# Kernel optimization log

Hardware: AMD Instinct MI355X
Metric: run time of the kernel (lower is better)

Reference implementation:

```python
import jax, jax.numpy as jnp
import numpy as np

EPS = 1e-10
TWO_PI = 2.0 * np.pi


def _nll(y_target, o_pred):
    # getCoef: split last dim of o_pred into 5 bivariate-Gaussian params
    mux = o_pred[..., 0]
    muy = o_pred[..., 1]
    sx = jnp.exp(o_pred[..., 2])
    sy = jnp.exp(o_pred[..., 3])
    corr = jnp.tanh(o_pred[..., 4])

    norm_x = (y_target[..., 1] - mux) / sx
    norm_y = (y_target[..., 2] - muy) / sy
    z = norm_x ** 2 + norm_y ** 2 - 2.0 * corr * norm_x * norm_y
    onemrho = 1.0 - corr ** 2
    top = jnp.exp(-z / (2.0 * onemrho))
    bottom = TWO_PI * (sx * sy * jnp.sqrt(onemrho))
    pdf = top / bottom  # (B, T, P)

    # sum over all (b, t, p) of -log(clamp(pdf, eps)), divided by ped_num
    total = jnp.sum(-jnp.log(jnp.clip(pdf, EPS)))
    return total / pdf.shape[2]


def setup_inputs() -> dict:
    key = jax.random.key(0)
    k1, k2 = jax.random.split(key)
    B, T, P = 64, 128, 512
    y_target = jax.random.normal(k1, (B, T, P, 3), dtype=jnp.float32)
    o_pred = jax.random.normal(k2, (B, T, P, 5), dtype=jnp.float32)
    return {"y_target": y_target, "o_pred": o_pred}


def reference(y_target, o_pred):
    return _nll(y_target, o_pred)
```

## Files before the change

kernel.cpp:

```cpp
#include <hip/hip_runtime.h>
#include <hip/hip_bf16.h>


#define THREADS 256
#define PPT 4
#define TILE (THREADS * PPT)

typedef float v4 __attribute__((ext_vector_type(4)));

__device__ __forceinline__ float point_nll(float mux, float muy, float lsx,
                                           float lsy, float w, float y1, float y2) {
    const float LOG_2PI = 1.8378770664093453f;
    const float CLIP    = 23.025850929940457f;
    float isx  = __expf(-lsx);
    float isy  = __expf(-lsy);
    float nx   = (y1 - mux) * isx;
    float ny   = (y2 - muy) * isy;
    float e2w  = __expf(2.0f * w);
    float corr = fmaf(-2.0f, __builtin_amdgcn_rcpf(e2w + 1.0f), 1.0f);
    float omr  = fmaf(-corr, corr, 1.0f);
    float z    = fmaf(nx, nx, ny * ny) - 2.0f * corr * nx * ny;
    float nll  = fmaf(z, 0.5f * __builtin_amdgcn_rcpf(omr),
                      fmaf(0.5f, __logf(omr), lsx + lsy + LOG_2PI));
    return fminf(nll, CLIP);
}

__global__ __launch_bounds__(THREADS) void nll_partial_kernel(
    const float* __restrict__ y, const float* __restrict__ o,
    float* __restrict__ partial, int N) {
    __shared__ v4 lds_o[5 * THREADS];
    __shared__ v4 lds_y[3 * THREADS];

    const int tid = threadIdx.x;
    const long long base_pt = (long long)blockIdx.x * TILE;
    float acc = 0.0f;

    if (base_pt + TILE <= (long long)N) {
        const v4* o4 = (const v4*)o + base_pt * 5 / 4;
        const v4* y4 = (const v4*)y + base_pt * 3 / 4;
#pragma unroll
        for (int k = 0; k < 5; ++k)
            lds_o[k * THREADS + tid] = __builtin_nontemporal_load(o4 + k * THREADS + tid);
#pragma unroll
        for (int k = 0; k < 3; ++k)
            lds_y[k * THREADS + tid] = __builtin_nontemporal_load(y4 + k * THREADS + tid);
        __syncthreads();

        const float* fo = (const float*)lds_o + tid * (PPT * 5);
        const float* fy = (const float*)lds_y + tid * (PPT * 3);
#pragma unroll
        for (int j = 0; j < PPT; ++j) {
            acc += point_nll(fo[5 * j + 0], fo[5 * j + 1], fo[5 * j + 2],
                             fo[5 * j + 3], fo[5 * j + 4],
                             fy[3 * j + 1], fy[3 * j + 2]);
        }
    } else {
        long long i0 = base_pt + (long long)tid * PPT;
        for (int j = 0; j < PPT; ++j) {
            long long i = i0 + j;
            if (i < (long long)N)
                acc += point_nll(o[i * 5 + 0], o[i * 5 + 1], o[i * 5 + 2],
                                 o[i * 5 + 3], o[i * 5 + 4],
                                 y[i * 3 + 1], y[i * 3 + 2]);
        }
    }

#pragma unroll
    for (int off = 32; off > 0; off >>= 1) acc += __shfl_down(acc, off, 64);
    __shared__ float ws[THREADS / 64];
    if ((tid & 63) == 0) ws[tid >> 6] = acc;
    __syncthreads();
    if (tid == 0) {
        float s = 0.0f;
#pragma unroll
        for (int i = 0; i < THREADS / 64; ++i) s += ws[i];
        partial[blockIdx.x] = s;
    }
}

__global__ __launch_bounds__(THREADS) void nll_final_kernel(
    const float* __restrict__ partial, int nparts, float* __restrict__ out,
    float inv_p) {
    float acc = 0.0f;
    for (int i = threadIdx.x; i < nparts; i += THREADS) acc += partial[i];
#pragma unroll
    for (int off = 32; off > 0; off >>= 1) acc += __shfl_down(acc, off, 64);
    __shared__ float ws[THREADS / 64];
    if ((threadIdx.x & 63) == 0) ws[threadIdx.x >> 6] = acc;
    __syncthreads();
    if (threadIdx.x == 0) {
        float s = 0.0f;
#pragma unroll
        for (int i = 0; i < THREADS / 64; ++i) s += ws[i];
        out[0] = s * inv_p;
    }
}

extern "C" void kernel_launch(void* const* d_in, const int* in_sizes, int n_in,
                              void* d_out, int out_size, void* d_ws, size_t ws_size,
                              hipStream_t stream) {
    const float* y = (const float*)d_in[0];
    const float* o = (const float*)d_in[1];
    int N = in_sizes[1] / 5;
    int blocks = (N + TILE - 1) / TILE;

    float* partial = (float*)d_ws;
    nll_partial_kernel<<<blocks, THREADS, 0, stream>>>(y, o, partial, N);
    nll_final_kernel<<<1, THREADS, 0, stream>>>(partial, blocks, (float*)d_out,
                                                1.0f / 512.0f);
}
```

Measured before the change: 151.8 us.

## Use persistent grid-stride blocks with register prefetch and per-wave LDS staging

Caps the grid at 1024 persistent blocks that stride over tiles. Each block prefetches the next tile's loads into registers while computing the current one. The LDS staging is split per wave so the block-wide __syncthreads before compute goes away, and the final reduction handles fewer partials. The aim is to overlap memory latency with compute on a bandwidth-bound reduction, at the cost of more registers and less occupancy.

```diff
diff --git a/kernel.cpp b/kernel.cpp
--- a/kernel.cpp
+++ b/kernel.cpp
@@ -5,6 +5,7 @@
 #define THREADS 256
 #define PPT 4
 #define TILE (THREADS * PPT)
+#define MAXBLOCKS 1024
 
 typedef float v4 __attribute__((ext_vector_type(4)));
 
@@ -28,47 +29,85 @@
 __global__ __launch_bounds__(THREADS) void nll_partial_kernel(
     const float* __restrict__ y, const float* __restrict__ o,
     float* __restrict__ partial, int N) {
-    __shared__ v4 lds_o[5 * THREADS];
-    __shared__ v4 lds_y[3 * THREADS];
+    __shared__ v4 lds[4][512];
+    const int tid  = threadIdx.x;
+    const int wave = tid >> 6;
+    const int lane = tid & 63;
+    v4* wbuf = lds[wave];
+    const v4* o4 = (const v4*)o;
+    const v4* y4 = (const v4*)y;
 
-    const int tid = threadIdx.x;
-    const long long base_pt = (long long)blockIdx.x * TILE;
+    const int ntiles = (N + TILE - 1) / TILE;
+    const int step   = gridDim.x;
     float acc = 0.0f;
 
-    if (base_pt + TILE <= (long long)N) {
-        const v4* o4 = (const v4*)o + base_pt * 5 / 4;
-        const v4* y4 = (const v4*)y + base_pt * 3 / 4;
+    int  t        = blockIdx.x;
+    bool valid    = t < ntiles;
+    bool cur_full = false;
+    v4 ro[5] = {}, ry[3] = {};
+    if (valid) {
+        cur_full = (long long)(t + 1) * TILE <= (long long)N;
+        if (cur_full) {
+            long long ob = (long long)t * 1280 + wave * 320 + lane;
+            long long yb = (long long)t * 768  + wave * 192 + lane;
 #pragma unroll
-        for (int k = 0; k < 5; ++k)
-            lds_o[k * THREADS + tid] = __builtin_nontemporal_load(o4 + k * THREADS + tid);
+            for (int k = 0; k < 5; ++k) ro[k] = __builtin_nontemporal_load(o4 + ob + k * 64);
 #pragma unroll
-        for (int k = 0; k < 3; ++k)
-            lds_y[k * THREADS + tid] = __builtin_nontemporal_load(y4 + k * THREADS + tid);
-        __syncthreads();
+            for (int k = 0; k < 3; ++k) ry[k] = __builtin_nontemporal_load(y4 + yb + k * 64);
+        }
+    }
 
-        const float* fo = (const float*)lds_o + tid * (PPT * 5);
-        const float* fy = (const float*)lds_y + tid * (PPT * 3);
+    while (valid) {
+        const int  tn     = t + step;
+        const bool nvalid = tn < ntiles;
+        const bool nfull  = nvalid && (long long)(tn + 1) * TILE <= (long long)N;
+        v4 po[5] = {}, py[3] = {};
+        if (nfull) {
+            long long ob = (long long)tn * 1280 + wave * 320 + lane;
+            long long yb = (long long)tn * 768  + wave * 192 + lane;
 #pragma unroll
-        for (int j = 0; j < PPT; ++j) {
-            acc += point_nll(fo[5 * j + 0], fo[5 * j + 1], fo[5 * j + 2],
-                             fo[5 * j + 3], fo[5 * j + 4],
-                             fy[3 * j + 1], fy[3 * j + 2]);
+            for (int k = 0; k < 5; ++k) po[k] = __builtin_nontemporal_load(o4 + ob + k * 64);
+#pragma unroll
+            for (int k = 0; k < 3; ++k) py[k] = __builtin_nontemporal_load(y4 + yb + k * 64);
         }
-    } else {
-        long long i0 = base_pt + (long long)tid * PPT;
-        for (int j = 0; j < PPT; ++j) {
-            long long i = i0 + j;
-            if (i < (long long)N)
-                acc += point_nll(o[i * 5 + 0], o[i * 5 + 1], o[i * 5 + 2],
-                                 o[i * 5 + 3], o[i * 5 + 4],
-                                 y[i * 3 + 1], y[i * 3 + 2]);
+
+        if (cur_full) {
+#pragma unroll
+            for (int k = 0; k < 5; ++k) wbuf[k * 64 + lane] = ro[k];
+#pragma unroll
+            for (int k = 0; k < 3; ++k) wbuf[320 + k * 64 + lane] = ry[k];
+            const float* fo = (const float*)wbuf + lane * (PPT * 5);
+            const float* fy = (const float*)(wbuf + 320) + lane * (PPT * 3);
+#pragma unroll
+            for (int j = 0; j < PPT; ++j) {
+                acc += point_nll(fo[5 * j + 0], fo[5 * j + 1], fo[5 * j + 2],
+                                 fo[5 * j + 3], fo[5 * j + 4],
+                                 fy[3 * j + 1], fy[3 * j + 2]);
+            }
+        } else {
+            long long base = (long long)t * TILE + wave * 256 + (long long)lane * PPT;
+            for (int j = 0; j < PPT; ++j) {
+                long long i = base + j;
+                if (i < (long long)N)
+                    acc += point_nll(o[i * 5 + 0], o[i * 5 + 1], o[i * 5 + 2],
+                                     o[i * 5 + 3], o[i * 5 + 4],
+                                     y[i * 3 + 1], y[i * 3 + 2]);
+            }
         }
+
+#pragma unroll
+        for (int k = 0; k < 5; ++k) ro[k] = po[k];
+#pragma unroll
+        for (int k = 0; k < 3; ++k) ry[k] = py[k];
+        cur_full = nfull;
+        t = tn;
+        valid = nvalid;
     }
 
 #pragma unroll
     for (int off = 32; off > 0; off >>= 1) acc += __shfl_down(acc, off, 64);
     __shared__ float ws[THREADS / 64];
-    if ((tid & 63) == 0) ws[tid >> 6] = acc;
+    if (lane == 0) ws[wave] = acc;
     __syncthreads();
     if (tid == 0) {
         float s = 0.0f;
@@ -102,7 +141,9 @@
     const float* y = (const float*)d_in[0];
     const float* o = (const float*)d_in[1];
     int N = in_sizes[1] / 5;
-    int blocks = (N + TILE - 1) / TILE;
+    int ntiles = (N + TILE - 1) / TILE;
+    int blocks = ntiles < MAXBLOCKS ? ntiles : MAXBLOCKS;
+    if (blocks < 1) blocks = 1;
 
     float* partial = (float*)d_ws;
     nll_partial_kernel<<<blocks, THREADS, 0, stream>>>(y, o, partial, N);
```

After: 150.7 us. Within noise of the previous version (-0.7%).

## Use persistent blocks with double-buffered direct-to-LDS global loads

Applied to the files above, without the earlier changes.

Replaces the one-tile-per-block launch with a persistent grid capped at 512 blocks that loops over tiles. Each wave loads its own slice straight into LDS with global_load_lds, double-buffered, and uses vmcnt waits instead of __syncthreads so the next tile's loads overlap compute on the current one. The aim is to hide memory latency and cut per-block launch and sync overhead on this bandwidth-bound reduction. The risks are the hand-coded waitcnt encodings, which are architecture-specific, and lower parallelism if 512 blocks cannot saturate HBM bandwidth.

```diff
diff --git a/kernel.cpp b/kernel.cpp
--- a/kernel.cpp
+++ b/kernel.cpp
@@ -5,8 +5,11 @@
 #define THREADS 256
 #define PPT 4
 #define TILE (THREADS * PPT)
+#define MAXBLOCKS 512
 
 typedef float v4 __attribute__((ext_vector_type(4)));
+typedef __attribute__((address_space(3))) v4 as3_v4;
+typedef const __attribute__((address_space(1))) v4 as1_v4;
 
 __device__ __forceinline__ float point_nll(float mux, float muy, float lsx,
                                            float lsy, float w, float y1, float y2) {
@@ -28,47 +31,68 @@
 __global__ __launch_bounds__(THREADS) void nll_partial_kernel(
     const float* __restrict__ y, const float* __restrict__ o,
     float* __restrict__ partial, int N) {
-    __shared__ v4 lds_o[5 * THREADS];
-    __shared__ v4 lds_y[3 * THREADS];
+    __shared__ v4 lds[4][2][512];
+    const int tid  = threadIdx.x;
+    const int wave = tid >> 6;
+    const int lane = tid & 63;
+    const v4* o4 = (const v4*)o;
+    const v4* y4 = (const v4*)y;
 
-    const int tid = threadIdx.x;
-    const long long base_pt = (long long)blockIdx.x * TILE;
+    const int nfull = N / TILE;
+    const int step  = gridDim.x;
     float acc = 0.0f;
 
-    if (base_pt + TILE <= (long long)N) {
-        const v4* o4 = (const v4*)o + base_pt * 5 / 4;
-        const v4* y4 = (const v4*)y + base_pt * 3 / 4;
+    auto issue = [&](int t, int b) {
+        const v4* gob = o4 + (long long)t * 1280 + wave * 320 + lane;
+        const v4* gyb = y4 + (long long)t * 768  + wave * 192 + lane;
+        v4* ob = &lds[wave][b][0];
+        v4* yb = &lds[wave][b][320];
 #pragma unroll
         for (int k = 0; k < 5; ++k)
-            lds_o[k * THREADS + tid] = __builtin_nontemporal_load(o4 + k * THREADS + tid);
+            __builtin_amdgcn_global_load_lds((as1_v4*)(gob + k * 64),
+                                             (as3_v4*)(ob + k * 64), 16, 0, 2 );
 #pragma unroll
         for (int k = 0; k < 3; ++k)
-            lds_y[k * THREADS + tid] = __builtin_nontemporal_load(y4 + k * THREADS + tid);
-        __syncthreads();
+            __builtin_amdgcn_global_load_lds((as1_v4*)(gyb + k * 64),
+                                             (as3_v4*)(yb + k * 64), 16, 0, 2 );
+    };
 
-        const float* fo = (const float*)lds_o + tid * (PPT * 5);
-        const float* fy = (const float*)lds_y + tid * (PPT * 3);
+    int t = blockIdx.x;
+    int p = 0;
+    if (t < nfull) issue(t, p);
+    while (t < nfull) {
+        const int  tn  = t + step;
+        const bool pre = tn < nfull;
+        if (pre) issue(tn, p ^ 1);
+
+        if (pre) __builtin_amdgcn_s_waitcnt(0x0F78);
+        else     __builtin_amdgcn_s_waitcnt(0x0F70);
+        asm volatile("" ::: "memory");
+
+        const float* fo = (const float*)&lds[wave][p][0]   + lane * (PPT * 5);
+        const float* fy = (const float*)&lds[wave][p][320] + lane * (PPT * 3);
 #pragma unroll
         for (int j = 0; j < PPT; ++j) {
             acc += point_nll(fo[5 * j + 0], fo[5 * j + 1], fo[5 * j + 2],
                              fo[5 * j + 3], fo[5 * j + 4],
                              fy[3 * j + 1], fy[3 * j + 2]);
         }
-    } else {
-        long long i0 = base_pt + (long long)tid * PPT;
-        for (int j = 0; j < PPT; ++j) {
-            long long i = i0 + j;
-            if (i < (long long)N)
-                acc += point_nll(o[i * 5 + 0], o[i * 5 + 1], o[i * 5 + 2],
-                                 o[i * 5 + 3], o[i * 5 + 4],
-                                 y[i * 3 + 1], y[i * 3 + 2]);
-        }
+        p ^= 1;
+        t = tn;
+    }
+
+    long long gid = (long long)blockIdx.x * THREADS + tid;
+    for (long long i = (long long)nfull * TILE + gid; i < (long long)N;
+         i += (long long)step * THREADS) {
+        acc += point_nll(o[i * 5 + 0], o[i * 5 + 1], o[i * 5 + 2],
+                         o[i * 5 + 3], o[i * 5 + 4],
+                         y[i * 3 + 1], y[i * 3 + 2]);
     }
 
 #pragma unroll
     for (int off = 32; off > 0; off >>= 1) acc += __shfl_down(acc, off, 64);
     __shared__ float ws[THREADS / 64];
-    if ((tid & 63) == 0) ws[tid >> 6] = acc;
+    if (lane == 0) ws[wave] = acc;
     __syncthreads();
     if (tid == 0) {
         float s = 0.0f;
@@ -102,7 +126,9 @@
     const float* y = (const float*)d_in[0];
     const float* o = (const float*)d_in[1];
     int N = in_sizes[1] / 5;
-    int blocks = (N + TILE - 1) / TILE;
+    int ntiles = (N + TILE - 1) / TILE;
+    int blocks = ntiles < MAXBLOCKS ? ntiles : MAXBLOCKS;
+    if (blocks < 1) blocks = 1;
 
     float* partial = (float*)d_ws;
     nll_partial_kernel<<<blocks, THREADS, 0, stream>>>(y, o, partial, N);
```

Result: no change. 149.7 us (-1.4%).
